# Kernel tuning notes

Measured on AMD Instinct MI355X. Metric: run time of the kernel, lower is better.

The kernel has to match this reference:

```python
import jax, jax.numpy as jnp
import numpy as np
from jax import lax


def extract_patches(x, kh, kw, sh, sw):
    # x: [B,H,W,C] -> [B,oh,ow,kh,kw,C], same element order as tf.image.extract_patches
    B, H, W, C = x.shape
    oh = (H - kh) // sh + 1
    ow = (W - kw) // sw + 1
    rows = jnp.arange(oh)[:, None] * sh + jnp.arange(kh)[None, :]  # [oh,kh]
    cols = jnp.arange(ow)[:, None] * sw + jnp.arange(kw)[None, :]  # [ow,kw]
    p = x[:, rows]            # [B,oh,kh,W,C]
    p = p[:, :, :, cols]      # [B,oh,kh,ow,kw,C]
    return jnp.transpose(p, (0, 1, 3, 2, 4, 5))  # [B,oh,ow,kh,kw,C]


def fastgrnn(x, W, U, bg, bu, zeta, nu):
    # FastGRNN: z=sigmoid(Wx+Uh+bg); c=tanh(Wx+Uh+bu); h'=z*h+(sig(zeta)*(1-z)+sig(nu))*c
    # x: [N,T,D] -> final hidden [N,H]
    wx = jnp.einsum('ntd,dh->nth', x, W)  # precompute input projection
    z_gate = jax.nn.sigmoid(zeta)
    n_gate = jax.nn.sigmoid(nu)

    def step(h, wx_t):
        pre = wx_t + h @ U
        z = jax.nn.sigmoid(pre + bg)
        c = jnp.tanh(pre + bu)
        h_new = z * h + (z_gate * (1.0 - z) + n_gate) * c
        return h_new, None

    h0 = jnp.zeros((x.shape[0], W.shape[1]), x.dtype)
    hT, _ = lax.scan(step, h0, jnp.swapaxes(wx, 0, 1))  # scan over T
    return hT


def rnnpool_forward(inputs, W1, U1, bg1, bu1, zeta1, nu1,
                    W2, U2, bg2, bu2, zeta2, nu2, kh, kw, sh, sw):
    B, H, Wd, C = inputs.shape
    oh = (H - kh) // sh + 1
    ow = (Wd - kw) // sw + 1
    patches = extract_patches(inputs, kh, kw, sh, sw)          # [B,oh,ow,kh,kw,C]
    N = B * oh * ow
    p = patches.reshape(N, kh, kw, C)

    u = W1.shape[1]
    # row-wise: rnn1 scans along cols within each row
    x = p.reshape(N * kh, kw, C)
    h = fastgrnn(x, W1, U1, bg1, bu1, zeta1, nu1).reshape(N, kh, u)
    o21 = fastgrnn(h, W2, U2, bg2, bu2, zeta2, nu2)
    o22 = fastgrnn(h[:, ::-1, :], W2, U2, bg2, bu2, zeta2, nu2)

    # col-wise: transpose patch, rnn1 scans along rows within each col
    xc = jnp.transpose(p, (0, 2, 1, 3)).reshape(N * kw, kh, C)
    hc = fastgrnn(xc, W1, U1, bg1, bu1, zeta1, nu1).reshape(N, kw, u)
    o23 = fastgrnn(hc, W2, U2, bg2, bu2, zeta2, nu2)
    o24 = fastgrnn(hc[:, ::-1, :], W2, U2, bg2, bu2, zeta2, nu2)

    out = jnp.concatenate([o21, o22, o23, o24], axis=1)        # [N, 4*hOut]
    return out.reshape(B, oh, ow, -1)


def setup_inputs() -> dict:
    key = jax.random.key(0)
    ks = jax.random.split(key, 9)
    C, u, hout = 16, 8, 16  # in-channels, rnn1 hidden, rnn2 hidden (out_channel//4)
    s = 0.1
    inp = {
        'inputs': jax.random.normal(ks[0], (32, 112, 112, C), jnp.float32),
        'W1': jax.random.normal(ks[1], (C, u), jnp.float32) * s,
        'U1': jax.random.normal(ks[2], (u, u), jnp.float32) * s,
        'bg1': jnp.ones((u,), jnp.float32),
        'bu1': jnp.ones((u,), jnp.float32),
        'zeta1': jnp.float32(100.0),
        'nu1': jnp.float32(-100.0),
        'W2': jax.random.normal(ks[3], (u, hout), jnp.float32) * s,
        'U2': jax.random.normal(ks[4], (hout, hout), jnp.float32) * s,
        'bg2': jnp.ones((hout,), jnp.float32),
        'bu2': jnp.ones((hout,), jnp.float32),
        'zeta2': jnp.float32(100.0),
        'nu2': jnp.float32(-100.0),
        'kh': 8, 'kw': 8, 'sh': 4, 'sw': 4,
    }
    return inp


def reference(inputs, W1, U1, bg1, bu1, zeta1, nu1,
              W2, U2, bg2, bu2, zeta2, nu2, kh, kw, sh, sw):
    return rnnpool_forward(inputs, W1, U1, bg1, bu1, zeta1, nu1,
                           W2, U2, bg2, bu2, zeta2, nu2, kh, kw, sh, sw)
```

## Files before the change

kernel.cpp:

```cpp
#include <hip/hip_runtime.h>

#define PPB 4

__device__ __forceinline__ float frcp(float x) { return __builtin_amdgcn_rcpf(x); }

__global__ __launch_bounds__(256, 4) void rnnpool_kernel(
    const float* __restrict__ inp,
    const float* __restrict__ W1, const float* __restrict__ U1,
    const float* __restrict__ bg1, const float* __restrict__ bu1,
    const float* __restrict__ zeta1, const float* __restrict__ nu1,
    const float* __restrict__ W2, const float* __restrict__ U2,
    const float* __restrict__ bg2, const float* __restrict__ bu2,
    const float* __restrict__ zeta2, const float* __restrict__ nu2,
    float* __restrict__ out)
{
  constexpr int C = 16, SH = 4, SW = 4;
  constexpr int OH = 27, OW = 27, HIN = 112, WIN = 112;
  constexpr int WXROW = 68;
  constexpr int HST = 12;
  constexpr int H2ST = 20;

  __shared__ float w1s[C * 8];
  __shared__ float wxs[PPB][8 * WXROW];
  __shared__ float hb[PPB][2][8 * HST];
  __shared__ float h2b[PPB][4 * H2ST];

  const int tid = threadIdx.x, wv = tid >> 6, lane = tid & 63;
  const int n = blockIdx.x * PPB + wv;
  const int pw = n % OW;
  const int q = n / OW;
  const int ph = q % OH, b = q / OH;

  if (tid < 32) ((float4*)w1s)[tid] = ((const float4*)W1)[tid];
  __syncthreads();

  const int r = lane >> 3, cpx = lane & 7;

  {
    const float* src = inp + (((size_t)(b * HIN + (ph * SH + r)) * WIN) + (pw * SW + cpx)) * C;
    float4 x0 = ((const float4*)src)[0], x1 = ((const float4*)src)[1],
           x2 = ((const float4*)src)[2], x3 = ((const float4*)src)[3];
    float xr[16] = {x0.x, x0.y, x0.z, x0.w, x1.x, x1.y, x1.z, x1.w,
                    x2.x, x2.y, x2.z, x2.w, x3.x, x3.y, x3.z, x3.w};
    float a0 = 0.f, a1 = 0.f, a2 = 0.f, a3 = 0.f, a4 = 0.f, a5 = 0.f, a6 = 0.f, a7 = 0.f;
#pragma unroll
    for (int ci = 0; ci < 16; ++ci) {
      float4 wA = *(const float4*)&w1s[ci * 8];
      float4 wB = *(const float4*)&w1s[ci * 8 + 4];
      a0 = fmaf(xr[ci], wA.x, a0);
      a1 = fmaf(xr[ci], wA.y, a1);
      a2 = fmaf(xr[ci], wA.z, a2);
      a3 = fmaf(xr[ci], wA.w, a3);
      a4 = fmaf(xr[ci], wB.x, a4);
      a5 = fmaf(xr[ci], wB.y, a5);
      a6 = fmaf(xr[ci], wB.z, a6);
      a7 = fmaf(xr[ci], wB.w, a7);
    }
    float* wd = &wxs[wv][r * WXROW + cpx * 8];
    *(float4*)wd = float4{a0, a1, a2, a3};
    *(float4*)(wd + 4) = float4{a4, a5, a6, a7};
  }
  __builtin_amdgcn_wave_barrier();

  const int seq = r, hid = cpx;
  float u1c[8];
#pragma unroll
  for (int i = 0; i < 8; ++i) u1c[i] = U1[i * 8 + hid];
  const float bg1v = bg1[hid], bu1v = bu1[hid];
  const float zg1 = frcp(1.f + __expf(-zeta1[0]));
  const float ng1 = frcp(1.f + __expf(-nu1[0]));
  const float A1 = zg1 + ng1;
  const float K1 = __expf(2.f * (bg1v - bu1v));

#pragma unroll
  for (int p = 0; p < 2; ++p) {
    float* hp = &hb[wv][p][0];
    float h;
    {
      float pre = (p == 0) ? wxs[wv][seq * WXROW + hid] : wxs[wv][seq * 8 + hid];
      float s = __expf(-(pre + bg1v));
      float z = frcp(1.f + s);
      float u = s * s * K1;
      float cc = fmaf(2.f, frcp(1.f + u), -1.f);
      float m = fmaf(-zg1, z, A1);
      h = m * cc;
      hp[seq * HST + hid] = h;
    }
    __builtin_amdgcn_wave_barrier();
#pragma unroll
    for (int t = 1; t < 8; ++t) {
      float4 h0 = *(const float4*)&hp[seq * HST];
      float4 h1 = *(const float4*)&hp[seq * HST + 4];
      float qa = h0.x * u1c[0], qb = h0.y * u1c[1];
      qa = fmaf(h0.z, u1c[2], qa);
      qb = fmaf(h0.w, u1c[3], qb);
      qa = fmaf(h1.x, u1c[4], qa);
      qb = fmaf(h1.y, u1c[5], qb);
      qa = fmaf(h1.z, u1c[6], qa);
      qb = fmaf(h1.w, u1c[7], qb);
      float wxv = (p == 0) ? wxs[wv][seq * WXROW + t * 8 + hid]
                           : wxs[wv][t * WXROW + seq * 8 + hid];
      float pre = wxv + qa + qb;
      float s = __expf(-(pre + bg1v));
      float z = frcp(1.f + s);
      float u = s * s * K1;
      float cc = fmaf(2.f, frcp(1.f + u), -1.f);
      float m = fmaf(-zg1, z, A1);
      h = fmaf(z, h, m * cc);
      hp[seq * HST + hid] = h;
      __builtin_amdgcn_wave_barrier();
    }
  }

  const int g = lane >> 4, j = lane & 15;
  float w2c[8], u2c[16];
#pragma unroll
  for (int d = 0; d < 8; ++d) w2c[d] = W2[d * 16 + j];
#pragma unroll
  for (int i = 0; i < 16; ++i) u2c[i] = U2[i * 16 + j];
  const float bg2v = bg2[j], bu2v = bu2[j];
  const float zg2 = frcp(1.f + __expf(-zeta2[0]));
  const float ng2 = frcp(1.f + __expf(-nu2[0]));
  const float A2 = zg2 + ng2;
  const float K2 = __expf(2.f * (bg2v - bu2v));
  const float* hsrc = &hb[wv][g >> 1][0];

  float h2;
  {
    const int tt = (g & 1) ? 7 : 0;
    const float4 a = *(const float4*)&hsrc[tt * HST];
    const float4 bq = *(const float4*)&hsrc[tt * HST + 4];
    float pa = a.x * w2c[0], pb = a.y * w2c[1];
    pa = fmaf(a.z, w2c[2], pa);
    pb = fmaf(a.w, w2c[3], pb);
    pa = fmaf(bq.x, w2c[4], pa);
    pb = fmaf(bq.y, w2c[5], pb);
    pa = fmaf(bq.z, w2c[6], pa);
    pb = fmaf(bq.w, w2c[7], pb);
    float pre = pa + pb;
    float s = __expf(-(pre + bg2v));
    float z = frcp(1.f + s);
    float u = s * s * K2;
    float cc = fmaf(2.f, frcp(1.f + u), -1.f);
    float m = fmaf(-zg2, z, A2);
    h2 = m * cc;
    h2b[wv][g * H2ST + j] = h2;
  }
  __builtin_amdgcn_wave_barrier();
#pragma unroll
  for (int t = 1; t < 8; ++t) {
    const int tt = (g & 1) ? (7 - t) : t;
    const float4 a = *(const float4*)&hsrc[tt * HST];
    const float4 bq = *(const float4*)&hsrc[tt * HST + 4];
    float pa = a.x * w2c[0], pb = a.y * w2c[1];
    pa = fmaf(a.z, w2c[2], pa);
    pb = fmaf(a.w, w2c[3], pb);
    pa = fmaf(bq.x, w2c[4], pa);
    pb = fmaf(bq.y, w2c[5], pb);
    pa = fmaf(bq.z, w2c[6], pa);
    pb = fmaf(bq.w, w2c[7], pb);

    const float* h2v = &h2b[wv][g * H2ST];
    const float4 v0 = *(const float4*)h2v;
    const float4 v1 = *(const float4*)(h2v + 4);
    const float4 v2 = *(const float4*)(h2v + 8);
    const float4 v3 = *(const float4*)(h2v + 12);
    float qa = v0.x * u2c[0], qb = v0.y * u2c[1];
    qa = fmaf(v0.z, u2c[2], qa);
    qb = fmaf(v0.w, u2c[3], qb);
    qa = fmaf(v1.x, u2c[4], qa);
    qb = fmaf(v1.y, u2c[5], qb);
    qa = fmaf(v1.z, u2c[6], qa);
    qb = fmaf(v1.w, u2c[7], qb);
    qa = fmaf(v2.x, u2c[8], qa);
    qb = fmaf(v2.y, u2c[9], qb);
    qa = fmaf(v2.z, u2c[10], qa);
    qb = fmaf(v2.w, u2c[11], qb);
    qa = fmaf(v3.x, u2c[12], qa);
    qb = fmaf(v3.y, u2c[13], qb);
    qa = fmaf(v3.z, u2c[14], qa);
    qb = fmaf(v3.w, u2c[15], qb);

    float pre = (pa + pb) + (qa + qb);
    float s = __expf(-(pre + bg2v));
    float z = frcp(1.f + s);
    float u = s * s * K2;
    float cc = fmaf(2.f, frcp(1.f + u), -1.f);
    float m = fmaf(-zg2, z, A2);
    h2 = fmaf(z, h2, m * cc);
    if (t < 7) {
      h2b[wv][g * H2ST + j] = h2;
      __builtin_amdgcn_wave_barrier();
    }
  }

  out[(size_t)n * 64 + lane] = h2;
}

extern "C" void kernel_launch(void* const* d_in, const int* in_sizes, int n_in,
                              void* d_out, int out_size, void* d_ws, size_t ws_size,
                              hipStream_t stream) {
  const float* inp   = (const float*)d_in[0];
  const float* W1    = (const float*)d_in[1];
  const float* U1    = (const float*)d_in[2];
  const float* bg1   = (const float*)d_in[3];
  const float* bu1   = (const float*)d_in[4];
  const float* zeta1 = (const float*)d_in[5];
  const float* nu1   = (const float*)d_in[6];
  const float* W2    = (const float*)d_in[7];
  const float* U2    = (const float*)d_in[8];
  const float* bg2   = (const float*)d_in[9];
  const float* bu2   = (const float*)d_in[10];
  const float* zeta2 = (const float*)d_in[11];
  const float* nu2   = (const float*)d_in[12];
  float* out = (float*)d_out;

  const int nblocks = 23328 / PPB;
  rnnpool_kernel<<<dim3(nblocks), dim3(256), 0, stream>>>(
      inp, W1, U1, bg1, bu1, zeta1, nu1, W2, U2, bg2, bu2, zeta2, nu2, out);
}
```

Baseline: 40.64 us.

## Split RNNPool into deduplicated layer-1 and layer-2 kernels through workspace

Overlapping 8x8 patches with stride 4 recompute the same first-layer row and column sequences several times. The first kernel now runs each distinct 8-long row or column FastGRNN sequence once and writes the final hidden states to workspace buffers. A second kernel gathers each patch's 8 row and 8 column states and runs the four second-layer scans. This roughly halves layer-1 compute and input reads. In exchange it adds a second launch and a global round trip of the intermediate states, with the old fused kernel kept as a fallback when the workspace is too small.

```diff
diff --git a/kernel.cpp b/kernel.cpp
--- a/kernel.cpp
+++ b/kernel.cpp
@@ -4,7 +4,231 @@
 
 __device__ __forceinline__ float frcp(float x) { return __builtin_amdgcn_rcpf(x); }
 
-__global__ __launch_bounds__(256, 4) void rnnpool_kernel(
+__global__ __launch_bounds__(256, 4) void l1_kernel(
+    const float* __restrict__ inp,
+    const float* __restrict__ W1, const float* __restrict__ U1,
+    const float* __restrict__ bg1, const float* __restrict__ bu1,
+    const float* __restrict__ zeta1, const float* __restrict__ nu1,
+    float* __restrict__ hrowg, float* __restrict__ hcolg)
+{
+  constexpr int C = 16, HIN = 112, WIN = 112;
+  constexpr int NROW = 32 * 14 * 27;
+  constexpr int WXROW = 68;
+  constexpr int HST = 12;
+
+  __shared__ float w1s[C * 8];
+  __shared__ float wxs[PPB][8 * WXROW];
+  __shared__ float hbuf[PPB][8 * HST];
+
+  const int tid = threadIdx.x, wv = tid >> 6, lane = tid & 63;
+  const int widx = blockIdx.x * PPB + wv;
+
+  if (tid < 32) ((float4*)w1s)[tid] = ((const float4*)W1)[tid];
+  __syncthreads();
+
+  const bool isrow = widx < NROW;
+  const int v = isrow ? widx : widx - NROW;
+  const int b = v / 378;
+  const int rem = v % 378;
+  const int t14 = rem / 27;
+  const int t27 = rem % 27;
+  const int ybase = isrow ? t14 * 8 : t27 * 4;
+  const int xbase = isrow ? t27 * 4 : t14 * 8;
+
+  const int r = lane >> 3, cpx = lane & 7;
+
+  {
+    const float* src = inp + (((size_t)(b * HIN + ybase + r) * WIN) + xbase + cpx) * C;
+    float4 x0 = ((const float4*)src)[0], x1 = ((const float4*)src)[1],
+           x2 = ((const float4*)src)[2], x3 = ((const float4*)src)[3];
+    float xr[16] = {x0.x, x0.y, x0.z, x0.w, x1.x, x1.y, x1.z, x1.w,
+                    x2.x, x2.y, x2.z, x2.w, x3.x, x3.y, x3.z, x3.w};
+    float a0 = 0.f, a1 = 0.f, a2 = 0.f, a3 = 0.f, a4 = 0.f, a5 = 0.f, a6 = 0.f, a7 = 0.f;
+#pragma unroll
+    for (int ci = 0; ci < 16; ++ci) {
+      float4 wA = *(const float4*)&w1s[ci * 8];
+      float4 wB = *(const float4*)&w1s[ci * 8 + 4];
+      a0 = fmaf(xr[ci], wA.x, a0);
+      a1 = fmaf(xr[ci], wA.y, a1);
+      a2 = fmaf(xr[ci], wA.z, a2);
+      a3 = fmaf(xr[ci], wA.w, a3);
+      a4 = fmaf(xr[ci], wB.x, a4);
+      a5 = fmaf(xr[ci], wB.y, a5);
+      a6 = fmaf(xr[ci], wB.z, a6);
+      a7 = fmaf(xr[ci], wB.w, a7);
+    }
+    float* wd = &wxs[wv][r * WXROW + cpx * 8];
+    *(float4*)wd = float4{a0, a1, a2, a3};
+    *(float4*)(wd + 4) = float4{a4, a5, a6, a7};
+  }
+  __builtin_amdgcn_wave_barrier();
+
+  const int seq = r, hid = cpx;
+  float u1c[8];
+#pragma unroll
+  for (int i = 0; i < 8; ++i) u1c[i] = U1[i * 8 + hid];
+  const float bg1v = bg1[hid], bu1v = bu1[hid];
+  const float zg1 = frcp(1.f + __expf(-zeta1[0]));
+  const float ng1 = frcp(1.f + __expf(-nu1[0]));
+  const float A1 = zg1 + ng1;
+  const float K1 = __expf(2.f * (bg1v - bu1v));
+
+  float* hp = &hbuf[wv][0];
+  float h;
+  auto run = [&](int off0, int step) {
+    {
+      float pre = wxs[wv][off0];
+      float s = __expf(-(pre + bg1v));
+      float z = frcp(1.f + s);
+      float u = s * s * K1;
+      float cc = fmaf(2.f, frcp(1.f + u), -1.f);
+      float m = fmaf(-zg1, z, A1);
+      h = m * cc;
+      hp[seq * HST + hid] = h;
+    }
+    __builtin_amdgcn_wave_barrier();
+#pragma unroll
+    for (int t = 1; t < 8; ++t) {
+      float4 h0 = *(const float4*)&hp[seq * HST];
+      float4 h1 = *(const float4*)&hp[seq * HST + 4];
+      float qa = h0.x * u1c[0], qb = h0.y * u1c[1];
+      qa = fmaf(h0.z, u1c[2], qa);
+      qb = fmaf(h0.w, u1c[3], qb);
+      qa = fmaf(h1.x, u1c[4], qa);
+      qb = fmaf(h1.y, u1c[5], qb);
+      qa = fmaf(h1.z, u1c[6], qa);
+      qb = fmaf(h1.w, u1c[7], qb);
+      float pre = wxs[wv][off0 + t * step] + qa + qb;
+      float s = __expf(-(pre + bg1v));
+      float z = frcp(1.f + s);
+      float u = s * s * K1;
+      float cc = fmaf(2.f, frcp(1.f + u), -1.f);
+      float m = fmaf(-zg1, z, A1);
+      h = fmaf(z, h, m * cc);
+      hp[seq * HST + hid] = h;
+      __builtin_amdgcn_wave_barrier();
+    }
+  };
+  if (isrow)
+    run(seq * WXROW + hid, 8);
+  else
+    run(seq * 8 + hid, WXROW);
+
+  const size_t oidx = (((size_t)(b * 27 + t27) * 112) + t14 * 8 + seq) * 8 + hid;
+  (isrow ? hrowg : hcolg)[oidx] = h;
+}
+
+__global__ __launch_bounds__(256, 4) void l2_kernel(
+    const float* __restrict__ hrowg, const float* __restrict__ hcolg,
+    const float* __restrict__ W2, const float* __restrict__ U2,
+    const float* __restrict__ bg2, const float* __restrict__ bu2,
+    const float* __restrict__ zeta2, const float* __restrict__ nu2,
+    float* __restrict__ out)
+{
+  constexpr int H2ST = 20;
+  __shared__ float hb[PPB][2][64];
+  __shared__ float h2b[PPB][4 * H2ST];
+
+  const int tid = threadIdx.x, wv = tid >> 6, lane = tid & 63;
+  const int n = blockIdx.x * PPB + wv;
+  const int pw = n % 27;
+  const int q = n / 27;
+  const int ph = q % 27, b = q / 27;
+
+  if (lane < 32) {
+    const int half = lane >> 4, idx = lane & 15;
+    const float* src = half ? &hcolg[(((size_t)(b * 27 + ph) * 112) + pw * 4) * 8]
+                            : &hrowg[(((size_t)(b * 27 + pw) * 112) + ph * 4) * 8];
+    ((float4*)&hb[wv][half][0])[idx] = ((const float4*)src)[idx];
+  }
+  __builtin_amdgcn_wave_barrier();
+
+  const int g = lane >> 4, j = lane & 15;
+  float w2c[8], u2c[16];
+#pragma unroll
+  for (int d = 0; d < 8; ++d) w2c[d] = W2[d * 16 + j];
+#pragma unroll
+  for (int i = 0; i < 16; ++i) u2c[i] = U2[i * 16 + j];
+  const float bg2v = bg2[j], bu2v = bu2[j];
+  const float zg2 = frcp(1.f + __expf(-zeta2[0]));
+  const float ng2 = frcp(1.f + __expf(-nu2[0]));
+  const float A2 = zg2 + ng2;
+  const float K2 = __expf(2.f * (bg2v - bu2v));
+  const float* hsrc = &hb[wv][g >> 1][0];
+
+  float h2;
+  {
+    const int tt = (g & 1) ? 7 : 0;
+    const float4 a = *(const float4*)&hsrc[tt * 8];
+    const float4 bq = *(const float4*)&hsrc[tt * 8 + 4];
+    float pa = a.x * w2c[0], pb = a.y * w2c[1];
+    pa = fmaf(a.z, w2c[2], pa);
+    pb = fmaf(a.w, w2c[3], pb);
+    pa = fmaf(bq.x, w2c[4], pa);
+    pb = fmaf(bq.y, w2c[5], pb);
+    pa = fmaf(bq.z, w2c[6], pa);
+    pb = fmaf(bq.w, w2c[7], pb);
+    float pre = pa + pb;
+    float s = __expf(-(pre + bg2v));
+    float z = frcp(1.f + s);
+    float u = s * s * K2;
+    float cc = fmaf(2.f, frcp(1.f + u), -1.f);
+    float m = fmaf(-zg2, z, A2);
+    h2 = m * cc;
+    h2b[wv][g * H2ST + j] = h2;
+  }
+  __builtin_amdgcn_wave_barrier();
+#pragma unroll
+  for (int t = 1; t < 8; ++t) {
+    const int tt = (g & 1) ? (7 - t) : t;
+    const float4 a = *(const float4*)&hsrc[tt * 8];
+    const float4 bq = *(const float4*)&hsrc[tt * 8 + 4];
+    float pa = a.x * w2c[0], pb = a.y * w2c[1];
+    pa = fmaf(a.z, w2c[2], pa);
+    pb = fmaf(a.w, w2c[3], pb);
+    pa = fmaf(bq.x, w2c[4], pa);
+    pb = fmaf(bq.y, w2c[5], pb);
+    pa = fmaf(bq.z, w2c[6], pa);
+    pb = fmaf(bq.w, w2c[7], pb);
+
+    const float* h2v = &h2b[wv][g * H2ST];
+    const float4 v0 = *(const float4*)h2v;
+    const float4 v1 = *(const float4*)(h2v + 4);
+    const float4 v2 = *(const float4*)(h2v + 8);
+    const float4 v3 = *(const float4*)(h2v + 12);
+    float qa = v0.x * u2c[0], qb = v0.y * u2c[1];
+    qa = fmaf(v0.z, u2c[2], qa);
+    qb = fmaf(v0.w, u2c[3], qb);
+    qa = fmaf(v1.x, u2c[4], qa);
+    qb = fmaf(v1.y, u2c[5], qb);
+    qa = fmaf(v1.z, u2c[6], qa);
+    qb = fmaf(v1.w, u2c[7], qb);
+    qa = fmaf(v2.x, u2c[8], qa);
+    qb = fmaf(v2.y, u2c[9], qb);
+    qa = fmaf(v2.z, u2c[10], qa);
+    qb = fmaf(v2.w, u2c[11], qb);
+    qa = fmaf(v3.x, u2c[12], qa);
+    qb = fmaf(v3.y, u2c[13], qb);
+    qa = fmaf(v3.z, u2c[14], qa);
+    qb = fmaf(v3.w, u2c[15], qb);
+
+    float pre = (pa + pb) + (qa + qb);
+    float s = __expf(-(pre + bg2v));
+    float z = frcp(1.f + s);
+    float u = s * s * K2;
+    float cc = fmaf(2.f, frcp(1.f + u), -1.f);
+    float m = fmaf(-zg2, z, A2);
+    h2 = fmaf(z, h2, m * cc);
+    if (t < 7) {
+      h2b[wv][g * H2ST + j] = h2;
+      __builtin_amdgcn_wave_barrier();
+    }
+  }
+
+  out[(size_t)n * 64 + lane] = h2;
+}
+
+__global__ __launch_bounds__(256, 4) void rnnpool_mono(
     const float* __restrict__ inp,
     const float* __restrict__ W1, const float* __restrict__ U1,
     const float* __restrict__ bg1, const float* __restrict__ bu1,
@@ -35,7 +259,6 @@
   __syncthreads();
 
   const int r = lane >> 3, cpx = lane & 7;
-
   {
     const float* src = inp + (((size_t)(b * HIN + (ph * SH + r)) * WIN) + (pw * SW + cpx)) * C;
     float4 x0 = ((const float4*)src)[0], x1 = ((const float4*)src)[1],
@@ -159,7 +382,6 @@
     pb = fmaf(bq.y, w2c[5], pb);
     pa = fmaf(bq.z, w2c[6], pa);
     pb = fmaf(bq.w, w2c[7], pb);
-
     const float* h2v = &h2b[wv][g * H2ST];
     const float4 v0 = *(const float4*)h2v;
     const float4 v1 = *(const float4*)(h2v + 4);
@@ -180,7 +402,6 @@
     qb = fmaf(v3.y, u2c[13], qb);
     qa = fmaf(v3.z, u2c[14], qa);
     qb = fmaf(v3.w, u2c[15], qb);
-
     float pre = (pa + pb) + (qa + qb);
     float s = __expf(-(pre + bg2v));
     float z = frcp(1.f + s);
@@ -193,7 +414,6 @@
       __builtin_amdgcn_wave_barrier();
     }
   }
-
   out[(size_t)n * 64 + lane] = h2;
 }
 
@@ -215,7 +435,16 @@
   const float* nu2   = (const float*)d_in[12];
   float* out = (float*)d_out;
 
-  const int nblocks = 23328 / PPB;
-  rnnpool_kernel<<<dim3(nblocks), dim3(256), 0, stream>>>(
-      inp, W1, U1, bg1, bu1, zeta1, nu1, W2, U2, bg2, bu2, zeta2, nu2, out);
+  const size_t HSZ = (size_t)32 * 27 * 112 * 8;
+  if (ws_size >= 2 * HSZ * sizeof(float)) {
+    float* hrowg = (float*)d_ws;
+    float* hcolg = hrowg + HSZ;
+    l1_kernel<<<dim3(6048), dim3(256), 0, stream>>>(
+        inp, W1, U1, bg1, bu1, zeta1, nu1, hrowg, hcolg);
+    l2_kernel<<<dim3(5832), dim3(256), 0, stream>>>(
+        hrowg, hcolg, W2, U2, bg2, bu2, zeta2, nu2, out);
+  } else {
+    rnnpool_mono<<<dim3(23328 / PPB), dim3(256), 0, stream>>>(
+        inp, W1, U1, bg1, bu1, zeta1, nu1, W2, U2, bg2, bu2, zeta2, nu2, out);
+  }
 }
```

After: 40.16 us. No clear change (-1.2%).
